# Kernel tuning notes

Hardware: AMD Instinct MI355X
Metric: run time of the kernel (lower is better)

Reference implementation:

```python
import jax, jax.numpy as jnp
import numpy as np

ALPHA = 32.0
EPS = 1e-8
NEG_SLOPE = 0.01  # torch F.leaky_relu default


def setup_inputs() -> dict:
    key = jax.random.key(0)
    k_x, k_h, k_a, k_b, k_c, k_d = jax.random.split(key, 6)
    B, S, D_IN, D_OUT, R = 4, 4096, 4096, 4096, 16
    std = 1.0 / np.sqrt(R)
    return {
        "x": jax.random.normal(k_x, (B, S, D_IN), dtype=jnp.float32),
        "h_t": jax.random.uniform(k_h, (B, S, R), dtype=jnp.float32),
        "W_a": jax.random.normal(k_a, (D_IN, R), dtype=jnp.float32) * std,
        "W_b": jax.random.normal(k_b, (R, D_OUT), dtype=jnp.float32) * std,
        "W_c": jax.random.normal(k_c, (R, R), dtype=jnp.float32) * std,
        "W_d": jax.random.normal(k_d, (R, R), dtype=jnp.float32) * std,
    }


def reference(x, h_t, W_a, W_b, W_c, W_d):
    # x: [B,S,in_dim]; h_t: [B,S,rank] (recurrent state already shape-matched)
    new_x = jnp.einsum("bsd,dr->bsr", x, W_a)            # [B,S,R]
    h_t1 = h_t @ W_c + new_x @ W_d + h_t                  # [B,S,R]
    # min-max normalization over the rank axis (dim=2)
    min_val = jnp.min(h_t1, axis=2, keepdims=True)
    max_val = jnp.max(h_t1, axis=2, keepdims=True)
    h_norm = (h_t1 - min_val) / (max_val - min_val + EPS)
    # dropout in eval mode (identity); leaky_relu with torch default slope
    act = jnp.where(h_norm >= 0, h_norm, NEG_SLOPE * h_norm)
    y = ALPHA * jnp.einsum("bsr,ro->bso", new_x + act, W_b)  # [B,S,out_dim]
    return y
```

## Files before the change

### kernel.cpp

```cpp
#include <hip/hip_runtime.h>

#define ALPHA_F 32.0f
#define EPS_F 1e-8f
#define NEG_SLOPE_F 0.01f

#define D_IN 4096
#define D_OUT 4096
#define RNK 16
#define N_ROWS 16384

__global__ __launch_bounds__(256) void wa_transpose(
    const float* __restrict__ Wa, float* __restrict__ WaT)
{
    const int idx = blockIdx.x * 256 + threadIdx.x;
    const int d = idx & (D_IN - 1);
    const int r = idx >> 12;
    WaT[idx] = Wa[d * RNK + r];
}

__global__ __launch_bounds__(256, 4) void ssm_stage1(
    const float* __restrict__ x,
    const float* __restrict__ h_t,
    const float* __restrict__ WaT,
    const float* __restrict__ Wc,
    const float* __restrict__ Wd,
    float* __restrict__ u)
{
    const int tid  = threadIdx.x;
    const int lane = tid & 63;
    const int w    = tid >> 6;
    const int g    = lane >> 4;
    const int q    = lane & 15;
    const long row = (long)blockIdx.x * 16 + w * 4 + g;

    const float4* x4  = (const float4*)x + row * (D_IN / 4);
    const float4* wt4 = (const float4*)WaT;

    float acc[RNK];
    #pragma unroll
    for (int r = 0; r < RNK; ++r) acc[r] = 0.0f;

    #pragma unroll 2
    for (int k = 0; k < 64; ++k) {
        const int p = q + (k << 4);
        const float4 xv = x4[p];
        #pragma unroll
        for (int r = 0; r < RNK; ++r) {
            const float4 wv = wt4[r * (D_IN / 4) + p];
            acc[r] += xv.x * wv.x + xv.y * wv.y + xv.z * wv.z + xv.w * wv.w;
        }
    }

    #pragma unroll
    for (int s = 0; s < 4; ++s) {
        const int m = 1 << s;
        const bool up = (lane & m) != 0;
        #pragma unroll
        for (int i = 0; i < (8 >> s); ++i) {
            const float a0 = acc[2 * i], a1 = acc[2 * i + 1];
            const float mine = up ? a1 : a0;
            const float send = up ? a0 : a1;
            acc[i] = mine + __shfl_xor(send, m, 64);
        }
    }
    const float nx = acc[0];

    const float h_own = h_t[row * RNK + q];
    float h1 = 0.0f;
    #pragma unroll
    for (int j = 0; j < RNK; ++j) {
        const float hj  = __shfl(h_own, j, 16);
        const float nxj = __shfl(nx, j, 16);
        const float wc  = Wc[j * RNK + q] + ((j == q) ? 1.0f : 0.0f);
        h1 += hj * wc + nxj * Wd[j * RNK + q];
    }

    float mn = h1, mx = h1;
    #pragma unroll
    for (int m = 1; m <= 8; m <<= 1) {
        mn = fminf(mn, __shfl_xor(mn, m, 64));
        mx = fmaxf(mx, __shfl_xor(mx, m, 64));
    }
    const float hn = (h1 - mn) / (mx - mn + EPS_F);
    const float a  = (hn >= 0.0f) ? hn : NEG_SLOPE_F * hn;
    u[row * RNK + q] = ALPHA_F * (nx + a);
}

__global__ __launch_bounds__(256) void ssm_stage2(
    const float* __restrict__ u,
    const float* __restrict__ Wb,
    float* __restrict__ y)
{
    const int tid  = threadIdx.x;
    const int lane = tid & 63;
    const int w    = tid >> 6;
    const long row0 = (long)blockIdx.x * 16 + w * 4;

    float4 uu[4][4];
    #pragma unroll
    for (int rr = 0; rr < 4; ++rr) {
        const float4* ur = (const float4*)(u + (row0 + rr) * RNK);
        #pragma unroll
        for (int j = 0; j < 4; ++j) uu[rr][j] = ur[j];
    }

    const float4* Wb4 = (const float4*)Wb;
    float4* y4 = (float4*)y;
    const long ybase = row0 * (D_OUT / 4);

    for (int k = 0; k < 16; ++k) {
        const int p = lane + (k << 6);
        float4 wb[16];
        #pragma unroll
        for (int r2 = 0; r2 < 16; ++r2) wb[r2] = Wb4[(size_t)r2 * 1024 + p];
        #pragma unroll
        for (int rr = 0; rr < 4; ++rr) {
            float4 o; o.x = 0.0f; o.y = 0.0f; o.z = 0.0f; o.w = 0.0f;
            #pragma unroll
            for (int r2 = 0; r2 < 16; ++r2) {
                const float us = ((const float*)&uu[rr][0])[r2];
                o.x += us * wb[r2].x;
                o.y += us * wb[r2].y;
                o.z += us * wb[r2].z;
                o.w += us * wb[r2].w;
            }
            y4[ybase + (long)rr * (D_OUT / 4) + p] = o;
        }
    }
}

__global__ __launch_bounds__(256) void ssm_lora_fused(
    const float* __restrict__ x,
    const float* __restrict__ h_t,
    const float* __restrict__ Wa,
    const float* __restrict__ Wb,
    const float* __restrict__ Wc,
    const float* __restrict__ Wd,
    float* __restrict__ y)
{
    __shared__ float red[4][16][68];
    __shared__ float lds_nx[16][16];
    __shared__ float lds_u[16][16];

    const int tid  = threadIdx.x;
    const int lane = tid & 63;
    const int w    = tid >> 6;
    const long row0 = (long)blockIdx.x * 16;
    const int wr0  = w * 4;

    float acc[4][16];
    #pragma unroll
    for (int rr = 0; rr < 4; ++rr)
        #pragma unroll
        for (int r = 0; r < 16; ++r) acc[rr][r] = 0.0f;

    const float4* x4 = (const float4*)x;
    const long xbase = (row0 + wr0) * (D_IN / 4);

    for (int k = 0; k < 16; ++k) {
        const int p = lane + (k << 6);
        float4 xv[4];
        #pragma unroll
        for (int rr = 0; rr < 4; ++rr)
            xv[rr] = x4[xbase + (long)rr * (D_IN / 4) + p];

        #pragma unroll
        for (int dd = 0; dd < 4; ++dd) {
            const float4* war = (const float4*)(Wa + ((size_t)(4 * p + dd) << 4));
            const float4 w0 = war[0], w1 = war[1], w2 = war[2], w3 = war[3];
            #pragma unroll
            for (int rr = 0; rr < 4; ++rr) {
                const float xs = ((const float*)&xv[rr])[dd];
                acc[rr][0]  += xs * w0.x;  acc[rr][1]  += xs * w0.y;
                acc[rr][2]  += xs * w0.z;  acc[rr][3]  += xs * w0.w;
                acc[rr][4]  += xs * w1.x;  acc[rr][5]  += xs * w1.y;
                acc[rr][6]  += xs * w1.z;  acc[rr][7]  += xs * w1.w;
                acc[rr][8]  += xs * w2.x;  acc[rr][9]  += xs * w2.y;
                acc[rr][10] += xs * w2.z;  acc[rr][11] += xs * w2.w;
                acc[rr][12] += xs * w3.x;  acc[rr][13] += xs * w3.y;
                acc[rr][14] += xs * w3.z;  acc[rr][15] += xs * w3.w;
            }
        }
    }

    #pragma unroll
    for (int rr = 0; rr < 4; ++rr)
        #pragma unroll
        for (int r = 0; r < 16; ++r) {
            float v = acc[rr][r];
            v += __shfl_xor(v, 1, 64);
            v += __shfl_xor(v, 2, 64);
            acc[rr][r] = v;
        }
    if ((lane & 3) == 0) {
        const int li = lane >> 2;
        #pragma unroll
        for (int rr = 0; rr < 4; ++rr)
            #pragma unroll
            for (int r = 0; r < 16; ++r)
                red[w][li][rr * 16 + r] = acc[rr][r];
    }
    __syncthreads();

    {
        const int row  = tid >> 4;
        const int r    = tid & 15;
        const int w2   = tid >> 6;
        const int slot = tid & 63;
        float s = 0.0f;
        #pragma unroll
        for (int i = 0; i < 16; ++i) s += red[w2][i][slot];
        lds_nx[row][r] = s;
        __syncthreads();

        const float* hrow = h_t + (row0 + row) * RNK;
        float h1 = hrow[r];
        #pragma unroll
        for (int j = 0; j < 16; ++j)
            h1 += hrow[j] * Wc[j * 16 + r] + lds_nx[row][j] * Wd[j * 16 + r];

        float mn = h1, mx = h1;
        #pragma unroll
        for (int m = 1; m <= 8; m <<= 1) {
            mn = fminf(mn, __shfl_xor(mn, m, 64));
            mx = fmaxf(mx, __shfl_xor(mx, m, 64));
        }
        const float hn = (h1 - mn) / (mx - mn + EPS_F);
        const float a  = (hn >= 0.0f) ? hn : NEG_SLOPE_F * hn;
        lds_u[row][r] = ALPHA_F * (s + a);
    }
    __syncthreads();

    float4 uu[4][4];
    #pragma unroll
    for (int rr = 0; rr < 4; ++rr)
        #pragma unroll
        for (int j = 0; j < 4; ++j)
            uu[rr][j] = ((const float4*)lds_u[wr0 + rr])[j];

    const float4* Wb4 = (const float4*)Wb;
    float4* y4 = (float4*)y;
    const long ybase = (row0 + wr0) * (D_OUT / 4);

    for (int k = 0; k < 16; ++k) {
        const int p = lane + (k << 6);
        float4 wb[16];
        #pragma unroll
        for (int r2 = 0; r2 < 16; ++r2) wb[r2] = Wb4[(size_t)r2 * 1024 + p];
        #pragma unroll
        for (int rr = 0; rr < 4; ++rr) {
            float4 o; o.x = 0.0f; o.y = 0.0f; o.z = 0.0f; o.w = 0.0f;
            #pragma unroll
            for (int r2 = 0; r2 < 16; ++r2) {
                const float us = ((const float*)&uu[rr][0])[r2];
                o.x += us * wb[r2].x;
                o.y += us * wb[r2].y;
                o.z += us * wb[r2].z;
                o.w += us * wb[r2].w;
            }
            y4[ybase + (long)rr * (D_OUT / 4) + p] = o;
        }
    }
}

extern "C" void kernel_launch(void* const* d_in, const int* in_sizes, int n_in,
                              void* d_out, int out_size, void* d_ws, size_t ws_size,
                              hipStream_t stream) {
    const float* x   = (const float*)d_in[0];
    const float* h_t = (const float*)d_in[1];
    const float* Wa  = (const float*)d_in[2];
    const float* Wb  = (const float*)d_in[3];
    const float* Wc  = (const float*)d_in[4];
    const float* Wd  = (const float*)d_in[5];
    float* y = (float*)d_out;

    const size_t need = (size_t)(RNK * D_IN + (size_t)N_ROWS * RNK) * sizeof(float);
    if (d_ws != nullptr && ws_size >= need) {
        float* WaT = (float*)d_ws;
        float* u   = WaT + (size_t)RNK * D_IN;
        wa_transpose<<<dim3((RNK * D_IN) / 256), dim3(256), 0, stream>>>(Wa, WaT);
        ssm_stage1<<<dim3(N_ROWS / 16), dim3(256), 0, stream>>>(x, h_t, WaT, Wc, Wd, u);
        ssm_stage2<<<dim3(N_ROWS / 16), dim3(256), 0, stream>>>(u, Wb, y);
    } else {
        ssm_lora_fused<<<dim3(N_ROWS / 16), dim3(256), 0, stream>>>(x, h_t, Wa, Wb, Wc, Wd, y);
    }
}
```

Baseline: 741.2 us.

## Fuse stage1 and stage2 into one kernel with register-prefetched x loads

Replaces the two-kernel path (stage1 writes u to global memory, stage2 reads it back) with one fused kernel per 16-row block. Each wave projects 4 rows against the transposed Wa with a one-step register prefetch of x, reduces partial sums through shuffles and LDS, computes the recurrence, normalization and activation in LDS, then does the Wb expansion. This removes the u round trip and one launch, and changes the reduction layout. In exchange it adds block-wide barriers and LDS use, and raises register pressure from the 4x16 accumulators plus prefetch buffers, which may lower occupancy.

```diff
diff --git a/kernel.cpp b/kernel.cpp
--- a/kernel.cpp
+++ b/kernel.cpp
@@ -8,6 +8,8 @@
 #define D_OUT 4096
 #define RNK 16
 #define N_ROWS 16384
+#define ROWS_PER_BLOCK 16
+#define THREADS 256
 
 __global__ __launch_bounds__(256) void wa_transpose(
     const float* __restrict__ Wa, float* __restrict__ WaT)
@@ -18,95 +20,129 @@
     WaT[idx] = Wa[d * RNK + r];
 }
 
-__global__ __launch_bounds__(256, 4) void ssm_stage1(
+__global__ __launch_bounds__(THREADS) void ssm_lora_fused_v2(
     const float* __restrict__ x,
     const float* __restrict__ h_t,
     const float* __restrict__ WaT,
+    const float* __restrict__ Wb,
     const float* __restrict__ Wc,
     const float* __restrict__ Wd,
-    float* __restrict__ u)
+    float* __restrict__ y)
 {
+    __shared__ float red[4][16][68];
+    __shared__ float lds_nx[16][16];
+    __shared__ float lds_u[16][16];
+
     const int tid  = threadIdx.x;
     const int lane = tid & 63;
     const int w    = tid >> 6;
-    const int g    = lane >> 4;
-    const int q    = lane & 15;
-    const long row = (long)blockIdx.x * 16 + w * 4 + g;
-
-    const float4* x4  = (const float4*)x + row * (D_IN / 4);
+    const long row0 = (long)blockIdx.x * ROWS_PER_BLOCK;
+    const int wr0  = w * 4;
+
+    float acc[4][16];
+    #pragma unroll
+    for (int rr = 0; rr < 4; ++rr)
+        #pragma unroll
+        for (int r = 0; r < 16; ++r) acc[rr][r] = 0.0f;
+
+    const float4* x4  = (const float4*)x;
     const float4* wt4 = (const float4*)WaT;
-
-    float acc[RNK];
-    #pragma unroll
-    for (int r = 0; r < RNK; ++r) acc[r] = 0.0f;
-
-    #pragma unroll 2
-    for (int k = 0; k < 64; ++k) {
-        const int p = q + (k << 4);
-        const float4 xv = x4[p];
-        #pragma unroll
-        for (int r = 0; r < RNK; ++r) {
-            const float4 wv = wt4[r * (D_IN / 4) + p];
-            acc[r] += xv.x * wv.x + xv.y * wv.y + xv.z * wv.z + xv.w * wv.w;
-        }
-    }
-
-    #pragma unroll
-    for (int s = 0; s < 4; ++s) {
-        const int m = 1 << s;
-        const bool up = (lane & m) != 0;
-        #pragma unroll
-        for (int i = 0; i < (8 >> s); ++i) {
-            const float a0 = acc[2 * i], a1 = acc[2 * i + 1];
-            const float mine = up ? a1 : a0;
-            const float send = up ? a0 : a1;
-            acc[i] = mine + __shfl_xor(send, m, 64);
-        }
-    }
-    const float nx = acc[0];
-
-    const float h_own = h_t[row * RNK + q];
-    float h1 = 0.0f;
-    #pragma unroll
-    for (int j = 0; j < RNK; ++j) {
-        const float hj  = __shfl(h_own, j, 16);
-        const float nxj = __shfl(nx, j, 16);
-        const float wc  = Wc[j * RNK + q] + ((j == q) ? 1.0f : 0.0f);
-        h1 += hj * wc + nxj * Wd[j * RNK + q];
-    }
-
-    float mn = h1, mx = h1;
-    #pragma unroll
-    for (int m = 1; m <= 8; m <<= 1) {
-        mn = fminf(mn, __shfl_xor(mn, m, 64));
-        mx = fmaxf(mx, __shfl_xor(mx, m, 64));
-    }
-    const float hn = (h1 - mn) / (mx - mn + EPS_F);
-    const float a  = (hn >= 0.0f) ? hn : NEG_SLOPE_F * hn;
-    u[row * RNK + q] = ALPHA_F * (nx + a);
-}
-
-__global__ __launch_bounds__(256) void ssm_stage2(
-    const float* __restrict__ u,
-    const float* __restrict__ Wb,
-    float* __restrict__ y)
-{
-    const int tid  = threadIdx.x;
-    const int lane = tid & 63;
-    const int w    = tid >> 6;
-    const long row0 = (long)blockIdx.x * 16 + w * 4;
+    const long xbase = (row0 + wr0) * (D_IN / 4);
+
+    float4 xv[4];
+    #pragma unroll
+    for (int rr = 0; rr < 4; ++rr)
+        xv[rr] = x4[xbase + (long)rr * (D_IN / 4) + lane];
+
+    for (int k = 0; k < 16; ++k) {
+        const int p = lane + (k << 6);
+        float4 xn[4];
+        if (k < 15) {
+            #pragma unroll
+            for (int rr = 0; rr < 4; ++rr)
+                xn[rr] = x4[xbase + (long)rr * (D_IN / 4) + p + 64];
+        }
+
+        #pragma unroll
+        for (int rh = 0; rh < 2; ++rh) {
+            float4 wv[8];
+            #pragma unroll
+            for (int r8 = 0; r8 < 8; ++r8)
+                wv[r8] = wt4[(size_t)(rh * 8 + r8) * (D_IN / 4) + p];
+            #pragma unroll
+            for (int r8 = 0; r8 < 8; ++r8) {
+                const int r = rh * 8 + r8;
+                #pragma unroll
+                for (int rr = 0; rr < 4; ++rr)
+                    acc[rr][r] += xv[rr].x * wv[r8].x + xv[rr].y * wv[r8].y
+                                + xv[rr].z * wv[r8].z + xv[rr].w * wv[r8].w;
+            }
+        }
+
+        if (k < 15) {
+            #pragma unroll
+            for (int rr = 0; rr < 4; ++rr) xv[rr] = xn[rr];
+        }
+    }
+
+    #pragma unroll
+    for (int rr = 0; rr < 4; ++rr)
+        #pragma unroll
+        for (int r = 0; r < 16; ++r) {
+            float v = acc[rr][r];
+            v += __shfl_xor(v, 1, 64);
+            v += __shfl_xor(v, 2, 64);
+            acc[rr][r] = v;
+        }
+    if ((lane & 3) == 0) {
+        const int li = lane >> 2;
+        #pragma unroll
+        for (int rr = 0; rr < 4; ++rr)
+            #pragma unroll
+            for (int r = 0; r < 16; ++r)
+                red[w][li][rr * 16 + r] = acc[rr][r];
+    }
+    __syncthreads();
+
+    {
+        const int row  = tid >> 4;
+        const int r    = tid & 15;
+        const int w2   = tid >> 6;
+        const int slot = tid & 63;
+        float s = 0.0f;
+        #pragma unroll
+        for (int i = 0; i < 16; ++i) s += red[w2][i][slot];
+        lds_nx[row][r] = s;
+        __syncthreads();
+
+        const float* hrow = h_t + (row0 + row) * RNK;
+        float h1 = hrow[r];
+        #pragma unroll
+        for (int j = 0; j < 16; ++j)
+            h1 += hrow[j] * Wc[j * 16 + r] + lds_nx[row][j] * Wd[j * 16 + r];
+
+        float mn = h1, mx = h1;
+        #pragma unroll
+        for (int m = 1; m <= 8; m <<= 1) {
+            mn = fminf(mn, __shfl_xor(mn, m, 64));
+            mx = fmaxf(mx, __shfl_xor(mx, m, 64));
+        }
+        const float hn = (h1 - mn) / (mx - mn + EPS_F);
+        const float a  = (hn >= 0.0f) ? hn : NEG_SLOPE_F * hn;
+        lds_u[row][r] = ALPHA_F * (s + a);
+    }
+    __syncthreads();
 
     float4 uu[4][4];
     #pragma unroll
-    for (int rr = 0; rr < 4; ++rr) {
-        const float4* ur = (const float4*)(u + (row0 + rr) * RNK);
-        #pragma unroll
-        for (int j = 0; j < 4; ++j) uu[rr][j] = ur[j];
-    }
+    for (int rr = 0; rr < 4; ++rr)
+        #pragma unroll
+        for (int j = 0; j < 4; ++j)
+            uu[rr][j] = ((const float4*)lds_u[wr0 + rr])[j];
 
     const float4* Wb4 = (const float4*)Wb;
     float4* y4 = (float4*)y;
-    const long ybase = row0 * (D_OUT / 4);
+    const long ybase = (row0 + wr0) * (D_OUT / 4);
 
     for (int k = 0; k < 16; ++k) {
         const int p = lane + (k << 6);
@@ -129,7 +165,7 @@
     }
 }
 
-__global__ __launch_bounds__(256) void ssm_lora_fused(
+__global__ __launch_bounds__(THREADS) void ssm_lora_fused(
     const float* __restrict__ x,
     const float* __restrict__ h_t,
     const float* __restrict__ Wa,
@@ -145,7 +181,7 @@
     const int tid  = threadIdx.x;
     const int lane = tid & 63;
     const int w    = tid >> 6;
-    const long row0 = (long)blockIdx.x * 16;
+    const long row0 = (long)blockIdx.x * ROWS_PER_BLOCK;
     const int wr0  = w * 4;
 
     float acc[4][16];
@@ -274,14 +310,14 @@
     const float* Wd  = (const float*)d_in[5];
     float* y = (float*)d_out;
 
-    const size_t need = (size_t)(RNK * D_IN + (size_t)N_ROWS * RNK) * sizeof(float);
+    const size_t need = (size_t)RNK * D_IN * sizeof(float);
+    dim3 grid(N_ROWS / ROWS_PER_BLOCK);
+    dim3 block(THREADS);
     if (d_ws != nullptr && ws_size >= need) {
         float* WaT = (float*)d_ws;
-        float* u   = WaT + (size_t)RNK * D_IN;
         wa_transpose<<<dim3((RNK * D_IN) / 256), dim3(256), 0, stream>>>(Wa, WaT);
-        ssm_stage1<<<dim3(N_ROWS / 16), dim3(256), 0, stream>>>(x, h_t, WaT, Wc, Wd, u);
-        ssm_stage2<<<dim3(N_ROWS / 16), dim3(256), 0, stream>>>(u, Wb, y);
+        ssm_lora_fused_v2<<<grid, block, 0, stream>>>(x, h_t, WaT, Wb, Wc, Wd, y);
     } else {
-        ssm_lora_fused<<<dim3(N_ROWS / 16), dim3(256), 0, stream>>>(x, h_t, Wa, Wb, Wc, Wd, y);
+        ssm_lora_fused<<<grid, block, 0, stream>>>(x, h_t, Wa, Wb, Wc, Wd, y);
     }
 }
```

New measurement: 638.5 us. -13.9%, faster.
